# Kernel optimization log

Hardware: AMD Instinct MI355X
Metric: run time of the kernel (lower is better)

The kernel has to match this reference:

```python
import jax, jax.numpy as jnp
import numpy as np

T_STEPS = 15          # SpykeTorch time dimension
THR1, THR2 = 15.0, 10.0   # conv1_threshold, conv2_threshold
KWTA2, RADIUS2 = 8, 1     # conv2_kwta, conv2_inhibition_radius


def conv2d(x, w):
    # F.conv2d, no padding, stride 1 (snn.Convolution)
    return jax.lax.conv_general_dilated(
        x, w, window_strides=(1, 1), padding='VALID',
        dimension_numbers=('NCHW', 'OIHW', 'NCHW'))


def maxpool(x, k, s):
    # sf.pooling == F.max_pool2d
    return jax.lax.reduce_window(x, -jnp.inf, jax.lax.max,
                                 (1, 1, k, k), (1, 1, s, s), 'VALID')


def fire(pot, thr):
    # sf.fire with return_thresholded_potentials=True
    pot_t = jnp.where(pot < thr, 0.0, pot)
    return jnp.sign(pot_t), pot_t


def pointwise_inhibition(pot):
    # sf.pointwise_inhibition: at each (h,w) keep only the feature that had the
    # max potential at the time of the earliest spike there.
    T, F, H, W = pot.shape
    max_vals = pot.max(axis=1, keepdims=True)            # (T,1,H,W)
    max_idx = pot.argmax(axis=1)                         # (T,H,W)
    clamp = jnp.sign(max_vals)                           # (T,1,H,W) 0/1 spike flag
    # earliest spike time per position (spikes are cumulative over T)
    earliest = jnp.clip((T - clamp.sum(axis=0)).astype(jnp.int32), 0, T - 1)  # (1,H,W)
    win_ch = jnp.take_along_axis(max_idx, earliest, axis=0)  # (1,H,W)
    # coef: one-hot over feature dim at winner channel, gated by spike at last step
    coef = (jnp.arange(F)[None, :, None, None] == win_ch[:, None, :, :]).astype(pot.dtype)
    coef = coef * clamp[-1:]                              # (1,F,H,W)
    return pot * coef


def get_k_winners(pot, spikes, kwta, radius):
    # sf.get_k_winners: rank by (earliest spike time, potential), then kwta
    # sequential suppression (same feature fully + spatial window, NMS-like).
    T, F, H, W = pot.shape
    first = jnp.clip((T - spikes.sum(axis=0, keepdims=True)).astype(jnp.int32), 0, T - 1)
    values = jnp.take_along_axis(pot, first, axis=0)      # (1,F,H,W)
    trunc = spikes * values
    v = trunc.max() * T                                   # big constant to prioritize early spikes
    total = (trunc + spikes * v).sum(axis=0)              # (F,H,W)
    fr = jnp.arange(F)[:, None, None]
    rr = jnp.arange(H)[None, :, None]
    cc = jnp.arange(W)[None, None, :]
    winners = []
    for _ in range(kwta):  # fixed small loop (kwta=8)
        idx = jnp.argmax(total)
        mx = total.reshape(-1)[idx]
        valid = mx != 0
        f = idx // (H * W)
        rem = idx % (H * W)
        r = rem // W
        c = rem % W
        winners.append(jnp.where(valid, jnp.stack([f, r, c]), -1))
        feat_hit = (fr == f)
        win_hit = (jnp.abs(rr - r) <= radius) & (jnp.abs(cc - c) <= radius)
        total = jnp.where(valid & (feat_hit | win_hit), 0.0, total)
    return jnp.stack(winners).astype(jnp.int32)           # (kwta,3)


def setup_inputs() -> dict:
    key = jax.random.key(0)
    k1, k2, k3 = jax.random.split(key, 3)
    inp = jax.random.randint(k1, (T_STEPS, 6, 160, 160), 0, 2, dtype=jnp.int32)
    # snn.Convolution weights ~ N(mean=0.8, std=0.05)
    w1 = 0.8 + 0.05 * jax.random.normal(k2, (30, 6, 5, 5), dtype=jnp.float32)
    w2 = 0.8 + 0.05 * jax.random.normal(k3, (250, 30, 3, 3), dtype=jnp.float32)
    return {"input": inp, "w1": w1, "w2": w2, "max_layer": 2}


def reference(input, w1, w2, max_layer):
    # Training-mode forward with max_layer == 2 (conv2 training branch).
    x = jnp.pad(input.astype(jnp.float32), ((0, 0), (0, 0), (2, 2), (2, 2)))
    pot = conv2d(x, w1)                                   # (15,30,160,160)
    spk, pot = fire(pot, THR1)
    spk_in = jnp.pad(maxpool(spk, 2, 2), ((0, 0), (0, 0), (1, 1), (1, 1)))
    pot = conv2d(spk_in, w2)                              # (15,250,80,80)
    spk, pot = fire(pot, THR2)
    pot = pointwise_inhibition(pot)
    spk = jnp.sign(pot)
    winners = get_k_winners(pot, spk, KWTA2, RADIUS2)
    return spk, pot, winners
```

## Files before the change

kernel.cpp:

```cpp
#include <hip/hip_runtime.h>


typedef unsigned short u16;
typedef unsigned char u8;
typedef __attribute__((ext_vector_type(8))) short short8;
typedef __attribute__((ext_vector_type(4))) float f32x4;
typedef __attribute__((ext_vector_type(4))) float float4v;

#define T_STEPS 15

#define INPCL_OFF   0u
#define SPKCL_OFF   6612480u
#define SPKROW_OFF  13067520u
#define W1CL_OFF    19119120u
#define WHI_OFF     19139600u
#define WLO_OFF     19287056u
#define MAXV_OFF    19434512u
#define ARGM_OFF    19818512u
#define WINMAP_OFF  20202512u
#define POTWIN_OFF  20228112u
#define CNT_OFF     20612112u
#define RSTHR_OFF   20813840u
#define RSMETA_OFF  20814864u

#define NB_REPACK 1615
#define NB_W1     40
#define NB_W2     288
#define NB_BORD   76
#define NB_BROW   18
#define NB_MISC   2
#define PREP_GRID (NB_REPACK + NB_W1 + NB_W2 + NB_BORD + NB_BROW + NB_MISC)

#define NB_CONV1  1500
#define NB_FILL   2048
#define K1B_GRID  (NB_CONV1 + NB_FILL)

#define NB_BMFMA  75
#define WS_GRID   (NB_BMFMA + 375)

static __device__ __forceinline__ u16 f2bf_rne(float f) {
  unsigned u = __float_as_uint(f);
  unsigned r = u + 0x7FFFu + ((u >> 16) & 1u);
  return (u16)(r >> 16);
}
static __device__ __forceinline__ float bf2f(u16 b) {
  return __uint_as_float(((unsigned)b) << 16);
}

static __device__ __forceinline__ void ring_decode(int r, int& h, int& w) {
  if (r < 80) { h = 0; w = r; }
  else if (r < 160) { h = 79; w = r - 80; }
  else if (r < 238) { h = 1 + (r - 160); w = 0; }
  else { h = 1 + (r - 238); w = 79; }
}

__global__ __launch_bounds__(256) void prep_kernel(
    const int* __restrict__ xin, const float* __restrict__ w1,
    const float* __restrict__ w2, u16* __restrict__ inp_cl,
    u16* __restrict__ w1cl, u16* __restrict__ Whi, u16* __restrict__ Wlo,
    u16* __restrict__ spk_cl, u16* __restrict__ spk_row,
    u16* __restrict__ cnt, float* __restrict__ rs_thr,
    float* __restrict__ rsmeta) {
  int tid = threadIdx.x, b = blockIdx.x;

  if (b < NB_REPACK) {
    int g = b * 256 + tid;
    if (g < 413280) {
      int t = g / 27552, rem = g % 27552;
      int yy = rem / 168, xx = rem % 168;
      int y = yy - 2, x = xx - 2;
      short8 sv = {0, 0, 0, 0, 0, 0, 0, 0};
      if ((unsigned)y < 160u && (unsigned)x < 160u) {
        const int* xb = xin + ((size_t)t * 6 * 160 + y) * 160 + x;
#pragma unroll
        for (int c = 0; c < 6; ++c)
          sv[c] = xb[c * 25600] ? (short)0x3F80 : (short)0;
      }
      *(short8*)(inp_cl + (size_t)g * 8) = sv;
    }
  } else if (b < NB_REPACK + NB_W1) {
    int idx = (b - NB_REPACK) * 256 + tid;
    int f = idx / 320, r = idx % 320;
    int ky = r / 64, r2 = r % 64;
    int kxb = r2 >> 5, k = r2 & 31;
    int dx = k >> 3, c = k & 7;
    int kx = kxb * 4 + dx;
    u16 v = 0;
    if (f < 30 && c < 6 && kx < 5)
      v = f2bf_rne(w1[(f * 6 + c) * 25 + ky * 5 + kx]);
    w1cl[idx] = v;
  } else if (b < NB_REPACK + NB_W1 + NB_W2) {
    int g2 = (b - NB_REPACK - NB_W1) * 256 + tid;
    int f = g2 / 288, r = g2 % 288;
    int kk = r >> 5, c = r & 31;
    u16 h = 0, l = 0;
    if (f < 250 && c < 30) {
      float w = w2[f * 270 + c * 9 + kk];
      h = f2bf_rne(w);
      l = f2bf_rne(w - bf2f(h));
    }
    Whi[g2] = h;
    Wlo[g2] = l;
  } else if (b < NB_REPACK + NB_W1 + NB_W2 + NB_BORD) {
    int u = (b - NB_REPACK - NB_W1 - NB_W2) * 256 + tid;
    if (u < 19440) {
      int pid = u >> 2, part = u & 3;
      int t = pid / 324, i = pid % 324;
      int row, col;
      if (i < 82) { row = 0; col = i; }
      else if (i < 164) { row = 81; col = i - 82; }
      else if (i < 244) { row = 1 + (i - 164); col = 0; }
      else { row = 1 + (i - 244); col = 81; }
      short8 z = {0, 0, 0, 0, 0, 0, 0, 0};
      *(short8*)(spk_cl + (((size_t)t * 82 + row) * 82 + col) * 32 +
                 part * 8) = z;
    }
  } else if (b < NB_REPACK + NB_W1 + NB_W2 + NB_BORD + NB_BROW) {
    int u0 = (b - NB_REPACK - NB_W1 - NB_W2 - NB_BORD) * 256 + tid;
    for (int v = u0; v < 145800; v += NB_BROW * 256) {
      int tc = v / 324, i = v % 324;
      int row, col;
      if (i < 82) { row = 0; col = i; }
      else if (i < 164) { row = 81; col = i - 82; }
      else if (i < 244) { row = 1 + (i - 164); col = 0; }
      else { row = 1 + (i - 244); col = 81; }
      spk_row[(size_t)tc * 6724 + row * 82 + col] = 0;
    }
  } else if (b == NB_REPACK + NB_W1 + NB_W2 + NB_BORD + NB_BROW) {
    __shared__ float sv[256];
    __shared__ int si[256];
    float a = 0.f;
    if (tid < 250) {
      const float* wt = w2 + tid * 270;
      for (int c = 0; c < 30; ++c)
#pragma unroll
        for (int kk = 0; kk < 9; ++kk)
          a = fmaf(wt[c * 9 + kk], 1.0f, a);
    }
    float thr = (a >= 10.f) ? a : 0.f;
    if (tid < 250) rs_thr[tid] = thr;
    sv[tid] = (tid < 250) ? thr : -1.f;
    si[tid] = tid;
    __syncthreads();
    for (int s = 128; s > 0; s >>= 1) {
      if (tid < s) {
        if (sv[tid + s] > sv[tid] ||
            (sv[tid + s] == sv[tid] && si[tid + s] < si[tid])) {
          sv[tid] = sv[tid + s];
          si[tid] = si[tid + s];
        }
      }
      __syncthreads();
    }
    if (tid == 0) {
      rsmeta[0] = sv[0];
      ((int*)rsmeta)[1] = si[0];
    }
  } else {
    for (int i = tid; i < 4860; i += 256) {
      int t = i / 324, r = i % 324;
      int row, col;
      if (r < 82) { row = 0; col = r; }
      else if (r < 164) { row = 81; col = r - 82; }
      else if (r < 244) { row = 1 + (r - 164); col = 0; }
      else { row = 1 + (r - 244); col = 81; }
      cnt[t * 6724 + row * 82 + col] = 0;
    }
  }
}

__global__ __launch_bounds__(256) void conv1_fill_kernel(
    const u16* __restrict__ inp_cl, const u16* __restrict__ w1cl,
    u16* __restrict__ spk_cl, u16* __restrict__ spk_row,
    u16* __restrict__ cnt, float4v* __restrict__ out4, int out_n4) {
  __shared__ u8 fires[30 * 256];
  __shared__ u16 pooled[64 * 32];

  int tid = threadIdx.x, b = blockIdx.x;

  if (b >= NB_CONV1) {
    int i = (b - NB_CONV1) * 256 + tid;
    float4v z = {0.f, 0.f, 0.f, 0.f};
    for (; i < out_n4; i += NB_FILL * 256) out4[i] = z;
    return;
  }

  int t = b / 100, tile = b % 100;
  int ty0 = (tile / 10) * 16, tx0 = (tile % 10) * 16;
  int lane = tid & 63, wave = tid >> 6, lrow = lane & 15, lgrp = lane >> 4;

  short8 afr[2][10];
#pragma unroll
  for (int mt = 0; mt < 2; ++mt)
#pragma unroll
    for (int s = 0; s < 10; ++s)
      afr[mt][s] =
          *(const short8*)(w1cl + ((mt * 16 + lrow) * 10 + s) * 32 + lgrp * 8);

  const u16* ib = inp_cl + (size_t)t * 164 * 168 * 8;

  for (int ph = 0; ph < 4; ++ph) {
    int rrow = ph * 4 + wave;
    int oy = ty0 + rrow;
    f32x4 acc0 = {0.f, 0.f, 0.f, 0.f}, acc1 = {0.f, 0.f, 0.f, 0.f};
#pragma unroll
    for (int s = 0; s < 10; ++s) {
      int ky = s >> 1, kxb = s & 1;
      short8 bfr = *(const short8*)(
          ib + (((oy + ky) * 168) + tx0 + lrow + kxb * 4 + lgrp) * 8);
      acc0 = __builtin_amdgcn_mfma_f32_16x16x32_bf16(afr[0][s], bfr, acc0,
                                                     0, 0, 0);
      acc1 = __builtin_amdgcn_mfma_f32_16x16x32_bf16(afr[1][s], bfr, acc1,
                                                     0, 0, 0);
    }
#pragma unroll
    for (int r = 0; r < 4; ++r) {
      int f0 = lgrp * 4 + r;
      fires[f0 * 256 + rrow * 16 + lrow] = (acc0[r] >= 15.f);
      int f1 = 16 + lgrp * 4 + r;
      if (f1 < 30) fires[f1 * 256 + rrow * 16 + lrow] = (acc1[r] >= 15.f);
    }
  }
  __syncthreads();

  int pby0 = (ty0 >> 1) + 1, pbx0 = (tx0 >> 1) + 1;

  for (int idx = tid; idx < 2048; idx += 256) {
    int f = idx >> 6, pp = idx & 63;
    int py = pp >> 3, px = pp & 7;
    u16 v = 0;
    if (f < 30) {
      const u8* fb = &fires[f * 256 + py * 32 + px * 2];
      v = (fb[0] | fb[1] | fb[16] | fb[17]) ? (u16)0x3F80 : (u16)0;
    }
    pooled[pp * 32 + f] = v;
  }
  for (int idx = tid; idx < 1920; idx += 256) {
    int f = idx >> 6, pp = idx & 63;
    int py = pp >> 3, px = pp & 7;
    const u8* fb = &fires[f * 256 + py * 32 + px * 2];
    u16 v = (fb[0] | fb[1] | fb[16] | fb[17]) ? (u16)0x3F80 : (u16)0;
    spk_row[((t * 30 + f) * 82 + pby0 + py) * 82 + pbx0 + px] = v;
  }
  __syncthreads();

  int pos = tid >> 2, part = tid & 3;
  int yy = pby0 + (pos >> 3), xx = pbx0 + (pos & 7);
  *(short8*)(spk_cl + (((size_t)t * 82 + yy) * 82 + xx) * 32 + part * 8) =
      *(short8*)&pooled[pos * 32 + part * 8];

  if (tid < 64) {
    int c = 0;
#pragma unroll
    for (int f = 0; f < 30; ++f) c += (pooled[tid * 32 + f] != 0) ? 1 : 0;
    cnt[t * 6724 + (pby0 + (tid >> 3)) * 82 + (pbx0 + (tid & 7))] = (u16)c;
  }
}

__global__ __launch_bounds__(256) void winsparse_kernel(
    const u16* __restrict__ spk_cl, const u16* __restrict__ spk_row,
    const u16* __restrict__ cnt, const u16* __restrict__ Whi,
    const u16* __restrict__ Wlo, const float* __restrict__ w2,
    const float* __restrict__ rsmeta, float* __restrict__ maxv_ws,
    int* __restrict__ argm_ws) {
  int tid = threadIdx.x, b = blockIdx.x;

  if (b >= NB_BMFMA) {
    int g = (b - NB_BMFMA) * 256 + tid;
    int t = g / 6400, pos = g % 6400;
    int h = pos / 80, w = pos % 80;
    if (h == 0 || h == 79 || w == 0 || w == 79) return;
    const u16* cb = cnt + t * 6724;
    int W = 0;
#pragma unroll
    for (int ky = 0; ky < 3; ++ky) {
      const u16* r = cb + (h + ky) * 82 + w;
      W += r[0] + r[1] + r[2];
    }
    if (W == 270) {
      maxv_ws[g] = rsmeta[0];
      argm_ws[g] = ((const int*)rsmeta)[1];
    } else {
      const u16* srb = spk_row + (size_t)t * 30 * 6724;
      float bv = -1.f; int bf = 0;
      for (int f = 0; f < 250; ++f) {
        const float* wt = w2 + f * 270;
        float a = 0.f;
        for (int c = 0; c < 30; ++c)
#pragma unroll
          for (int ky = 0; ky < 3; ++ky)
#pragma unroll
            for (int kx = 0; kx < 3; ++kx)
              a = fmaf(wt[c * 9 + ky * 3 + kx],
                       bf2f(srb[c * 6724 + (h + ky) * 82 + (w + kx)]), a);
        float v = (a >= 10.f) ? a : 0.f;
        if (v > bv) { bv = v; bf = f; }
      }
      maxv_ws[g] = bv;
      argm_ws[g] = bf;
    }
    return;
  }

  __shared__ __align__(16) u16 Xt[64 * 320];
  __shared__ int eid[64];

  if (tid < 64) {
    int e = b * 64 + tid;
    if (e >= 4740) e = 4739;
    int t = e / 316, r = e % 316;
    int h, w;
    ring_decode(r, h, w);
    eid[tid] = t * 6400 + h * 80 + w;
  }
  __syncthreads();

  for (int task = tid; task < 2304; task += 256) {
    int e = task / 36, r = task % 36;
    int kk = r >> 2, part = r & 3;
    int g = eid[e];
    int t = g / 6400, pos = g % 6400;
    int h = pos / 80, w = pos % 80;
    int ky = kk / 3, kx = kk % 3;
    short8 v = *(const short8*)(
        spk_cl + (((size_t)t * 82 + h + ky) * 82 + (w + kx)) * 32 + part * 8);
    int off = (e * 320 + kk * 32 + part * 8) ^ ((e & 7) << 3);
    *(short8*)(Xt + off) = v;
  }
  __syncthreads();

  int lane = tid & 63, wave = tid >> 6, lrow = lane & 15, lgrp = lane >> 4;
  int fbase = wave * 64;

  f32x4 acc[4][4];
#pragma unroll
  for (int i = 0; i < 4; ++i)
#pragma unroll
    for (int j = 0; j < 4; ++j) acc[i][j] = (f32x4){0.f, 0.f, 0.f, 0.f};

  const u16* whib = Whi + (fbase + lrow) * 288 + lgrp * 8;
  const u16* wlob = Wlo + (fbase + lrow) * 288 + lgrp * 8;
  int xorr = (lrow & 7) << 3;

#pragma unroll
  for (int ks = 0; ks < 9; ++ks) {
    short8 ahi[4], alo[4], bfr[4];
#pragma unroll
    for (int ft = 0; ft < 4; ++ft) {
      ahi[ft] = *(const short8*)(whib + ft * 16 * 288 + ks * 32);
      alo[ft] = *(const short8*)(wlob + ft * 16 * 288 + ks * 32);
    }
#pragma unroll
    for (int pt = 0; pt < 4; ++pt) {
      int s = ((pt * 16 + lrow) * 320 + ks * 32 + lgrp * 8) ^ xorr;
      bfr[pt] = *(const short8*)(Xt + s);
    }
#pragma unroll
    for (int ft = 0; ft < 4; ++ft)
#pragma unroll
      for (int pt = 0; pt < 4; ++pt) {
        acc[ft][pt] = __builtin_amdgcn_mfma_f32_16x16x32_bf16(
            ahi[ft], bfr[pt], acc[ft][pt], 0, 0, 0);
        acc[ft][pt] = __builtin_amdgcn_mfma_f32_16x16x32_bf16(
            alo[ft], bfr[pt], acc[ft][pt], 0, 0, 0);
      }
  }

  __syncthreads();
  float* redv = (float*)Xt;
  int* redi = (int*)(Xt + 512);

#pragma unroll
  for (int pt = 0; pt < 4; ++pt) {
    float bv = -1.f; int bf = 0;
#pragma unroll
    for (int ft = 0; ft < 4; ++ft)
#pragma unroll
      for (int r = 0; r < 4; ++r) {
        float v = acc[ft][pt][r];
        v = (v >= 10.f) ? v : 0.f;
        int f = fbase + ft * 16 + lgrp * 4 + r;
        if (v > bv) { bv = v; bf = f; }
      }
    {
      float ov = __shfl_xor(bv, 16); int of = __shfl_xor(bf, 16);
      if (ov > bv || (ov == bv && of < bf)) { bv = ov; bf = of; }
      ov = __shfl_xor(bv, 32); of = __shfl_xor(bf, 32);
      if (ov > bv || (ov == bv && of < bf)) { bv = ov; bf = of; }
    }
    if (lgrp == 0) {
      redv[wave * 64 + pt * 16 + lrow] = bv;
      redi[wave * 64 + pt * 16 + lrow] = bf;
    }
  }
  __syncthreads();
  if (tid < 64) {
    float bv = -1.f; int bf = 0x7fffffff;
#pragma unroll
    for (int w = 0; w < 4; ++w) {
      float v = redv[w * 64 + tid]; int f = redi[w * 64 + tid];
      if (v > bv || (v == bv && f < bf)) { bv = v; bf = f; }
    }
    int g = eid[tid];
    maxv_ws[g] = bv;
    argm_ws[g] = bf;
  }
}

__global__ __launch_bounds__(256) void recompute_kernel(
    const u16* __restrict__ spk_row, const float* __restrict__ w2,
    const u16* __restrict__ cnt, const float* __restrict__ rs_thr,
    const float* __restrict__ maxv, const int* __restrict__ argm,
    int* __restrict__ winmap, float* __restrict__ potwin) {
  __shared__ u16 patch[30 * 18 * 18];
  __shared__ int anyp;

  int tid = threadIdx.x, b = blockIdx.x;
  int t = b / 25, tile = b % 25;
  int ty0 = (tile / 5) * 16, tx0 = (tile % 5) * 16;
  int py = tid >> 4, px = tid & 15;
  int h = ty0 + py, w = tx0 + px;
  int pos = h * 80 + w;

  const u16* cb = cnt + t * 6724;
  int W = 0;
#pragma unroll
  for (int ky = 0; ky < 3; ++ky) {
    const u16* r = cb + (h + ky) * 82 + w;
    W += r[0] + r[1] + r[2];
  }
  int partial = (W != 270);
  if (tid == 0) anyp = 0;
  __syncthreads();
  if (partial) anyp = 1;
  __syncthreads();
  int do_stage = anyp;

  if (do_stage) {
    const u16* base = spk_row + (size_t)t * 30 * 6724;
    unsigned* p32 = (unsigned*)patch;
    for (int idx = tid; idx < 4860; idx += 256) {
      int c = idx / 162, rem = idx % 162;
      int dy = rem / 9, dxp = rem % 9;
      p32[idx] = *(const unsigned*)(base + c * 6724 + (ty0 + dy) * 82 + tx0 +
                                    dxp * 2);
    }
  }

  int nc = 0;
#pragma unroll
  for (int tt = 0; tt < T_STEPS; ++tt)
    nc += (maxv[tt * 6400 + pos] > 0.f) ? 1 : 0;
  int e = T_STEPS - nc; if (e > 14) e = 14;
  int win = argm[e * 6400 + pos];
  if (!(maxv[14 * 6400 + pos] > 0.f)) win = -1;
  if (t == 0) winmap[pos] = win;

  if (do_stage) __syncthreads();

  float p = 0.f;
  if (win >= 0) {
    if (!partial) {
      p = rs_thr[win];
    } else {
      const float* wt = w2 + win * 270;
      float a = 0.f;
      for (int c = 0; c < 30; ++c) {
#pragma unroll
        for (int ky = 0; ky < 3; ++ky)
#pragma unroll
          for (int kx = 0; kx < 3; ++kx)
            a = fmaf(wt[c * 9 + ky * 3 + kx],
                     bf2f(patch[c * 324 + (py + ky) * 18 + (px + kx)]), a);
      }
      p = (a >= 10.f) ? a : 0.f;
    }
  }
  potwin[t * 6400 + pos] = p;
}

__global__ __launch_bounds__(1024) void finalize_kernel(
    const int* __restrict__ winmap, const float* __restrict__ potwin,
    float* __restrict__ out, float* __restrict__ out_win) {
  __shared__ float tv[6400];
  __shared__ int   tf[6400];
  __shared__ float wv_s[16];
  __shared__ int   wk_s[16];
  __shared__ int   sh_w[4];
  __shared__ float vmax_s;

  int tid = threadIdx.x;
  int b = blockIdx.x;

  if (b > 0) {
    int pos = (b - 1) * 256 + (tid & 255);
    int tq = tid >> 8;
    int win = winmap[pos];
    if (win < 0) return;
    int tend = tq * 4 + 4; if (tend > T_STEPS) tend = T_STEPS;
    for (int t = tq * 4; t < tend; ++t) {
      float p = potwin[t * 6400 + pos];
      int o = (t * 250 + win) * 6400 + pos;
      out[o] = (p > 0.f) ? 1.f : 0.f;
      out[24000000 + o] = p;
    }
    return;
  }

  int lane = tid & 63, wid = tid >> 6;

  float localmax = 0.f;
  for (int pos = tid; pos < 6400; pos += 1024) {
    int win = winmap[pos];
    float val = 0.f; int nspk = 0;
    if (win >= 0) {
#pragma unroll
      for (int t = 0; t < T_STEPS; ++t)
        nspk += (potwin[t * 6400 + pos] > 0.f) ? 1 : 0;
      int first = T_STEPS - nspk; if (first > 14) first = 14;
      val = potwin[first * 6400 + pos];
      if (nspk > 0 && val > localmax) localmax = val;
    }
    tv[pos] = val;
    tf[pos] = ((win + 1) << 4) | nspk;
  }
#pragma unroll
  for (int m = 1; m < 64; m <<= 1)
    localmax = fmaxf(localmax, __shfl_xor(localmax, m));
  if (lane == 0) wv_s[wid] = localmax;
  __syncthreads();
  if (tid == 0) {
    float m = 0.f;
#pragma unroll
    for (int w = 0; w < 16; ++w) m = fmaxf(m, wv_s[w]);
    vmax_s = m * (float)T_STEPS;
  }
  __syncthreads();
  float v = vmax_s;

  for (int pos = tid; pos < 6400; pos += 1024) {
    int meta = tf[pos];
    int win = (meta >> 4) - 1, nspk = meta & 15;
    tf[pos] = win;
    tv[pos] = (win >= 0) ? (float)nspk * (tv[pos] + v) : 0.f;
  }
  __syncthreads();

  for (int it = 0; it < 8; ++it) {
    float bv = -1.f; int bk = 0x7fffffff;
    for (int pos = tid; pos < 6400; pos += 1024) {
      float tvv = tv[pos];
      int key = tf[pos] * 6400 + pos;
      if (tvv > bv || (tvv == bv && key < bk)) { bv = tvv; bk = key; }
    }
#pragma unroll
    for (int m = 1; m < 64; m <<= 1) {
      float ov = __shfl_xor(bv, m); int ok = __shfl_xor(bk, m);
      if (ov > bv || (ov == bv && ok < bk)) { bv = ov; bk = ok; }
    }
    if (lane == 0) { wv_s[wid] = bv; wk_s[wid] = bk; }
    __syncthreads();
    if (tid == 0) {
      float mbv = -1.f; int mbk = 0x7fffffff;
#pragma unroll
      for (int w = 0; w < 16; ++w) {
        float ov = wv_s[w]; int ok = wk_s[w];
        if (ov > mbv || (ov == mbv && ok < mbk)) { mbv = ov; mbk = ok; }
      }
      int f = -1, r = -1, c = -1, valid = 0;
      if (mbv != 0.f) {
        f = mbk / 6400; int pos = mbk % 6400;
        r = pos / 80; c = pos % 80;
        valid = 1;
      }
      out_win[it * 3 + 0] = (float)f;
      out_win[it * 3 + 1] = (float)r;
      out_win[it * 3 + 2] = (float)c;
      sh_w[0] = f; sh_w[1] = r; sh_w[2] = c; sh_w[3] = valid;
    }
    __syncthreads();
    if (sh_w[3]) {
      int wf = sh_w[0], wr = sh_w[1], wc = sh_w[2];
      for (int pos = tid; pos < 6400; pos += 1024) {
        int r = pos / 80, c = pos % 80;
        int dr = r - wr; if (dr < 0) dr = -dr;
        int dc = c - wc; if (dc < 0) dc = -dc;
        if (tf[pos] == wf || (dr <= 1 && dc <= 1)) tv[pos] = 0.f;
      }
    }
    __syncthreads();
  }
}

extern "C" void kernel_launch(void* const* d_in, const int* in_sizes, int n_in,
                              void* d_out, int out_size, void* d_ws,
                              size_t ws_size, hipStream_t stream) {
  const int*   xin = (const int*)d_in[0];
  const float* w1  = (const float*)d_in[1];
  const float* w2  = (const float*)d_in[2];
  float* out = (float*)d_out;
  char*  ws  = (char*)d_ws;

  u16*   inp_cl  = (u16*)(ws + INPCL_OFF);
  u16*   spk_cl  = (u16*)(ws + SPKCL_OFF);
  u16*   spk_row = (u16*)(ws + SPKROW_OFF);
  u16*   w1cl    = (u16*)(ws + W1CL_OFF);
  u16*   Whi     = (u16*)(ws + WHI_OFF);
  u16*   Wlo     = (u16*)(ws + WLO_OFF);
  float* maxv    = (float*)(ws + MAXV_OFF);
  int*   argm    = (int*)(ws + ARGM_OFF);
  int*   winmap  = (int*)(ws + WINMAP_OFF);
  float* potwin  = (float*)(ws + POTWIN_OFF);
  u16*   cnt     = (u16*)(ws + CNT_OFF);
  float* rs_thr  = (float*)(ws + RSTHR_OFF);
  float* rsmeta  = (float*)(ws + RSMETA_OFF);

  prep_kernel<<<PREP_GRID, 256, 0, stream>>>(xin, w1, w2, inp_cl, w1cl, Whi,
                                             Wlo, spk_cl, spk_row, cnt,
                                             rs_thr, rsmeta);
  conv1_fill_kernel<<<K1B_GRID, 256, 0, stream>>>(inp_cl, w1cl, spk_cl,
                                                  spk_row, cnt,
                                                  (float4v*)d_out,
                                                  out_size / 4);
  winsparse_kernel<<<WS_GRID, 256, 0, stream>>>(spk_cl, spk_row, cnt, Whi,
                                                Wlo, w2, rsmeta, maxv, argm);
  recompute_kernel<<<375, 256, 0, stream>>>(spk_row, w2, cnt, rs_thr, maxv,
                                            argm, winmap, potwin);
  finalize_kernel<<<26, 1024, 0, stream>>>(winmap, potwin, out,
                                           out + 48000000);
}
```

Before: 136.7 us.

## Split output zero-fill across conv1 and winsparse kernels with interleaved block roles

The zeroing of the large output buffer is split into two parts. The first part stays in the conv1 kernel and the remainder moves into the winsparse kernel, so the memory-bound fill overlaps with two compute phases instead of one. Compute and fill blocks are interleaved by block index parity so both roles are dispatched together rather than fill blocks trailing at the end of the grid. This adds shared-memory allocation to the fill blocks in the winsparse kernel, which may lower occupancy, and hardcodes the split point in the output.

```diff
diff --git a/kernel.cpp b/kernel.cpp
--- a/kernel.cpp
+++ b/kernel.cpp
@@ -32,11 +32,14 @@
 #define PREP_GRID (NB_REPACK + NB_W1 + NB_W2 + NB_BORD + NB_BROW + NB_MISC)
 
 #define NB_CONV1  1500
-#define NB_FILL   2048
-#define K1B_GRID  (NB_CONV1 + NB_FILL)
+#define NB_FILLA  1536
+#define FILLA_N4  9000000
+#define K2_GRID   3036
 
 #define NB_BMFMA  75
-#define WS_GRID   (NB_BMFMA + 375)
+#define NB_WS     450
+#define NB_FILLB  512
+#define K3_GRID   962
 
 static __device__ __forceinline__ u16 f2bf_rne(float f) {
   unsigned u = __float_as_uint(f);
@@ -172,20 +175,24 @@
 __global__ __launch_bounds__(256) void conv1_fill_kernel(
     const u16* __restrict__ inp_cl, const u16* __restrict__ w1cl,
     u16* __restrict__ spk_cl, u16* __restrict__ spk_row,
-    u16* __restrict__ cnt, float4v* __restrict__ out4, int out_n4) {
+    u16* __restrict__ cnt, float4v* __restrict__ out4) {
   __shared__ u8 fires[30 * 256];
   __shared__ u16 pooled[64 * 32];
 
   int tid = threadIdx.x, b = blockIdx.x;
 
-  if (b >= NB_CONV1) {
-    int i = (b - NB_CONV1) * 256 + tid;
+  int role, idx;
+  if (b < 3000) { role = b & 1; idx = b >> 1; }
+  else { role = 1; idx = 1500 + (b - 3000); }
+
+  if (role == 1) {
+    int i = idx * 256 + tid;
     float4v z = {0.f, 0.f, 0.f, 0.f};
-    for (; i < out_n4; i += NB_FILL * 256) out4[i] = z;
+    for (; i < FILLA_N4; i += NB_FILLA * 256) out4[i] = z;
     return;
   }
 
-  int t = b / 100, tile = b % 100;
+  int t = idx / 100, tile = idx % 100;
   int ty0 = (tile / 10) * 16, tx0 = (tile % 10) * 16;
   int lane = tid & 63, wave = tid >> 6, lrow = lane & 15, lgrp = lane >> 4;
 
@@ -225,8 +232,8 @@
 
   int pby0 = (ty0 >> 1) + 1, pbx0 = (tx0 >> 1) + 1;
 
-  for (int idx = tid; idx < 2048; idx += 256) {
-    int f = idx >> 6, pp = idx & 63;
+  for (int idx2 = tid; idx2 < 2048; idx2 += 256) {
+    int f = idx2 >> 6, pp = idx2 & 63;
     int py = pp >> 3, px = pp & 7;
     u16 v = 0;
     if (f < 30) {
@@ -235,8 +242,8 @@
     }
     pooled[pp * 32 + f] = v;
   }
-  for (int idx = tid; idx < 1920; idx += 256) {
-    int f = idx >> 6, pp = idx & 63;
+  for (int idx2 = tid; idx2 < 1920; idx2 += 256) {
+    int f = idx2 >> 6, pp = idx2 & 63;
     int py = pp >> 3, px = pp & 7;
     const u8* fb = &fires[f * 256 + py * 32 + px * 2];
     u16 v = (fb[0] | fb[1] | fb[16] | fb[17]) ? (u16)0x3F80 : (u16)0;
@@ -257,16 +264,30 @@
   }
 }
 
-__global__ __launch_bounds__(256) void winsparse_kernel(
+__global__ __launch_bounds__(256) void winsparse_fill_kernel(
     const u16* __restrict__ spk_cl, const u16* __restrict__ spk_row,
     const u16* __restrict__ cnt, const u16* __restrict__ Whi,
     const u16* __restrict__ Wlo, const float* __restrict__ w2,
     const float* __restrict__ rsmeta, float* __restrict__ maxv_ws,
-    int* __restrict__ argm_ws) {
+    int* __restrict__ argm_ws, float4v* __restrict__ out4, int out_n4) {
+  __shared__ __align__(16) u16 Xt[64 * 320];
+  __shared__ int eid[64];
+
   int tid = threadIdx.x, b = blockIdx.x;
 
-  if (b >= NB_BMFMA) {
-    int g = (b - NB_BMFMA) * 256 + tid;
+  int role, idx;
+  if (b < 900) { role = b & 1; idx = b >> 1; }
+  else { role = 1; idx = 450 + (b - 900); }
+
+  if (role == 1) {
+    int i = FILLA_N4 + idx * 256 + tid;
+    float4v z = {0.f, 0.f, 0.f, 0.f};
+    for (; i < out_n4; i += NB_FILLB * 256) out4[i] = z;
+    return;
+  }
+
+  if (idx >= NB_BMFMA) {
+    int g = (idx - NB_BMFMA) * 256 + tid;
     int t = g / 6400, pos = g % 6400;
     int h = pos / 80, w = pos % 80;
     if (h == 0 || h == 79 || w == 0 || w == 79) return;
@@ -302,11 +323,8 @@
     return;
   }
 
-  __shared__ __align__(16) u16 Xt[64 * 320];
-  __shared__ int eid[64];
-
   if (tid < 64) {
-    int e = b * 64 + tid;
+    int e = idx * 64 + tid;
     if (e >= 4740) e = 4739;
     int t = e / 316, r = e % 316;
     int h, w;
@@ -618,12 +636,12 @@
   prep_kernel<<<PREP_GRID, 256, 0, stream>>>(xin, w1, w2, inp_cl, w1cl, Whi,
                                              Wlo, spk_cl, spk_row, cnt,
                                              rs_thr, rsmeta);
-  conv1_fill_kernel<<<K1B_GRID, 256, 0, stream>>>(inp_cl, w1cl, spk_cl,
-                                                  spk_row, cnt,
-                                                  (float4v*)d_out,
-                                                  out_size / 4);
-  winsparse_kernel<<<WS_GRID, 256, 0, stream>>>(spk_cl, spk_row, cnt, Whi,
-                                                Wlo, w2, rsmeta, maxv, argm);
+  conv1_fill_kernel<<<K2_GRID, 256, 0, stream>>>(inp_cl, w1cl, spk_cl,
+                                                 spk_row, cnt,
+                                                 (float4v*)d_out);
+  winsparse_fill_kernel<<<K3_GRID, 256, 0, stream>>>(
+      spk_cl, spk_row, cnt, Whi, Wlo, w2, rsmeta, maxv, argm,
+      (float4v*)d_out, out_size / 4);
   recompute_kernel<<<375, 256, 0, stream>>>(spk_row, w2, cnt, rs_thr, maxv,
                                             argm, winmap, potwin);
   finalize_kernel<<<26, 1024, 0, stream>>>(winmap, potwin, out,
```

After: 141.4 us. 1.03x slower.
